# Kernel optimization log

Hardware: AMD Instinct MI355X
Metric: run time of the kernel (lower is better)

## Reference

```python
import jax, jax.numpy as jnp
import numpy as np

N_SIDE = 64
P = N_SIDE * N_SIDE          # n_patch = 4096
B = 8                        # n_batch
H = 32                       # n_hidden
E = H + 2                    # mhsa embed_dim = 34
N_OBS = 10
N_PRED = 50


def _neighbor_flat():
    # Reproduce the module's boundary-corrected 3x3 neighborhood indices.
    idx = np.arange(P)
    rows, cols = idx // N_SIDE, idx % N_SIDE
    off = np.array([[-1, -1], [-1, 0], [-1, 1], [0, -1], [0, 0], [0, 1], [1, -1], [1, 0], [1, 1]])
    nr = (rows[:, None] + off[:, 0]).reshape(N_SIDE, N_SIDE, 9)
    nc = (cols[:, None] + off[:, 1]).reshape(N_SIDE, N_SIDE, 9)
    nr[0] += 1; nr[-1] -= 1          # shift edge rows inward
    nc[:, 0] += 1; nc[:, -1] -= 1    # shift edge cols inward
    return jnp.asarray((nr * N_SIDE + nc).reshape(P, 9))

NEIGH = _neighbor_flat()  # (P, 9) flat patch indices


def _patch_label():
    r = (np.arange(N_SIDE) / N_SIDE).astype(np.float32)
    lab = np.stack(np.meshgrid(r, r, indexing='ij'), axis=-1).reshape(P, 2)
    return jnp.asarray(lab)

LABEL = _patch_label()  # (P, 2) normalized (row, col) coords


def _layernorm(x, g, b, eps=1e-5):
    m = x.mean(-1, keepdims=True)
    v = ((x - m) ** 2).mean(-1, keepdims=True)
    return (x - m) * jax.lax.rsqrt(v + eps) * g + b


def _step(h, params):
    # One local-attention step: h (B*P, H) -> layernorm(fc2(h + fc_sa(attn_center)))
    ipw, ipb, opw, opb, saw, sab, f2w, f2b, lg, lb = params
    q = h.reshape(B, P, H).transpose(1, 0, 2)                       # (P, B, H)
    lab = jnp.broadcast_to(LABEL[:, None, :], (P, B, 2))
    q = jnp.concatenate([q, lab], axis=-1)                          # (P, B, E)
    tok = q[NEIGH]                                                  # (P, 9, B, E) neighbor gather
    tok = tok.transpose(1, 2, 0, 3).reshape(9, B * P, E)            # (S=9, N, E)
    qkv = tok @ ipw.T + ipb                                         # (9, N, 3E)
    qq, kk, vv = jnp.split(qkv, 3, axis=-1)
    scores = jnp.einsum('sne,tne->nst', qq, kk) / jnp.sqrt(jnp.float32(E))
    w = jax.nn.softmax(scores, axis=-1)                             # (N, 9, 9)
    av = jnp.einsum('nst,tne->sne', w, vv)                          # (9, N, E)
    av = av @ opw.T + opb
    new_h = h + av[4] @ saw.T + sab                                 # center token + residual
    return _layernorm(new_h @ f2w.T + f2b, lg, lb)


def setup_inputs() -> dict:
    key = jax.random.key(0)
    ks = jax.random.split(key, 10)
    s = 0.05
    return {
        'x': jax.random.normal(ks[0], (N_OBS, B * P, H), jnp.float32),
        'in_proj_w': jax.random.normal(ks[1], (3 * E, E), jnp.float32) * s,
        'in_proj_b': jax.random.normal(ks[2], (3 * E,), jnp.float32) * s,
        'out_proj_w': jax.random.normal(ks[3], (E, E), jnp.float32) * s,
        'out_proj_b': jax.random.normal(ks[4], (E,), jnp.float32) * s,
        'fc_sa_w': jax.random.normal(ks[5], (H, E), jnp.float32) * s,
        'fc_sa_b': jax.random.normal(ks[6], (H,), jnp.float32) * s,
        'fc2_w': jax.random.normal(ks[7], (H, H), jnp.float32) * s,
        'fc2_b': jax.random.normal(ks[8], (H,), jnp.float32) * s,
        'ln2_g': jnp.ones((H,), jnp.float32),
        'ln2_b': jnp.zeros((H,), jnp.float32),
    }


def reference(x, in_proj_w, in_proj_b, out_proj_w, out_proj_b, fc_sa_w, fc_sa_b, fc2_w, fc2_b, ln2_g, ln2_b):
    params = (in_proj_w, in_proj_b, out_proj_w, out_proj_b, fc_sa_w, fc_sa_b, fc2_w, fc2_b, ln2_g, ln2_b)
    # Observation phase: 10 independent steps over x[t] -> vmap over time.
    obs = jax.vmap(lambda xt: _step(xt, params))(x)                 # (N_OBS, N, H)
    # Prediction phase: 50 sequential steps rolling on the last prediction.
    def scan_fn(h, _):
        p = _step(h, params)
        return p, p
    _, preds = jax.lax.scan(scan_fn, obs[-1], None, length=N_PRED)  # (N_PRED, N, H)
    return jnp.concatenate([obs, preds], axis=0)                    # (60, B*P, H)
```

## Files before the change

### kernel.cpp

```cpp
#include <hip/hip_runtime.h>
#include <hip/hip_bf16.h>

typedef __hip_bfloat16 bf16;
typedef unsigned short u16;
typedef unsigned int   u32;

#define PP    4096
#define HH    32
#define NTOK  32768
#define NSTEP 60
#define NOBS  10
#define SKK   35
#define SVP   33

#define OFF_WIN  0
#define OFF_BIN  3672
#define OFF_WFSA 3776
#define OFF_BFSA 4928
#define OFF_F2W  4960
#define OFF_F2B  5984
#define OFF_LNG  6016
#define OFF_LNB  6048
#define OFF_WVP  6080
#define OFF_BVP  7232
#define WGT_FLOATS 7264
#define WGT_BYTES  (7296 * 4)

__device__ __forceinline__ float bb(bf16 v) { return __bfloat162float(v); }

__device__ __forceinline__ int detect_f32(const u16* raw) {
  int bad = 0;
#pragma unroll
  for (int i = 0; i < 40; i++) {
    float f = __uint_as_float(((u32)raw[2 * i]) << 16);
    bad |= !(fabsf(f) < 1.0f);
  }
  return bad;
}

__device__ __forceinline__ float rdw(const void* p, int i, int f32) {
  return f32 ? ((const float*)p)[i] : bb(((const bf16*)p)[i]);
}

__device__ __forceinline__ void load_h(const void* hsrc, int hf32, int n, float* he) {
  if (hf32) {
    const float4* p = (const float4*)((const float*)hsrc + (size_t)n * HH);
#pragma unroll
    for (int k = 0; k < 8; k++) {
      float4 v = p[k];
      he[4 * k] = v.x; he[4 * k + 1] = v.y; he[4 * k + 2] = v.z; he[4 * k + 3] = v.w;
    }
  } else {
    const uint4* p = (const uint4*)((const bf16*)hsrc + (size_t)n * HH);
#pragma unroll
    for (int k = 0; k < 4; k++) {
      uint4 v = p[k];
      u32 w[4] = {v.x, v.y, v.z, v.w};
#pragma unroll
      for (int m = 0; m < 4; m++) {
        he[8 * k + 2 * m]     = __uint_as_float(w[m] << 16);
        he[8 * k + 2 * m + 1] = __uint_as_float(w[m] & 0xffff0000u);
      }
    }
  }
}

__device__ __forceinline__ void load_h8(const void* hsrc, int hf32, int n, int off, float* o8) {
  if (hf32) {
    const float4* p = (const float4*)((const float*)hsrc + (size_t)n * HH + off);
    float4 a = p[0], b = p[1];
    o8[0]=a.x; o8[1]=a.y; o8[2]=a.z; o8[3]=a.w;
    o8[4]=b.x; o8[5]=b.y; o8[6]=b.z; o8[7]=b.w;
  } else {
    uint4 v = *(const uint4*)((const bf16*)hsrc + (size_t)n * HH + off);
    u32 w[4] = {v.x, v.y, v.z, v.w};
#pragma unroll
    for (int m = 0; m < 4; m++) {
      o8[2 * m]     = __uint_as_float(w[m] << 16);
      o8[2 * m + 1] = __uint_as_float(w[m] & 0xffff0000u);
    }
  }
}

__global__ void prep_kernel(const void* __restrict__ ipw, const void* __restrict__ ipb,
                            const void* __restrict__ opw, const void* __restrict__ opb,
                            const void* __restrict__ saw, const void* __restrict__ sab,
                            const void* __restrict__ f2w, const void* __restrict__ f2b,
                            const void* __restrict__ lng, const void* __restrict__ lnb,
                            float* __restrict__ gw) {
  const int f32 = detect_f32((const u16*)ipw);
  int i = blockIdx.x * blockDim.x + threadIdx.x;
  if (i < 3672) { int r = i / 36, e = i - r * 36;
    gw[OFF_WIN + i] = (e < 34) ? rdw(ipw, r * 34 + e, f32) : 0.f; return; }
  i -= 3672;
  if (i < 104)  { gw[OFF_BIN + i] = (i < 102) ? rdw(ipb, i, f32) : 0.f; return; }
  i -= 104;
  if (i < 1152) { int r = i / 36, e = i - r * 36; float a = 0.f;
    if (e < 34) for (int f = 0; f < 34; f++)
      a += rdw(saw, r * 34 + f, f32) * rdw(opw, f * 34 + e, f32);
    gw[OFF_WFSA + i] = a; return; }
  i -= 1152;
  if (i < 32)   { float a = rdw(sab, i, f32);
    for (int f = 0; f < 34; f++) a += rdw(saw, i * 34 + f, f32) * rdw(opb, f, f32);
    gw[OFF_BFSA + i] = a; return; }
  i -= 32;
  if (i < 1024) { gw[OFF_F2W + i] = rdw(f2w, i, f32); return; }
  i -= 1024;
  if (i < 32)   { gw[OFF_F2B + i] = rdw(f2b, i, f32); return; }
  i -= 32;
  if (i < 32)   { gw[OFF_LNG + i] = rdw(lng, i, f32); return; }
  i -= 32;
  if (i < 32)   { gw[OFF_LNB + i] = rdw(lnb, i, f32); return; }
  i -= 32;
  if (i < 1152) {
    int r = i / 36, e = i - r * 36; float a = 0.f;
    if (e < 34) {
      for (int f = 0; f < 34; f++) {
        float wf = 0.f;
        for (int g = 0; g < 34; g++)
          wf += rdw(saw, r * 34 + g, f32) * rdw(opw, g * 34 + f, f32);
        a += wf * rdw(ipw, (68 + f) * 34 + e, f32);
      }
    }
    gw[OFF_WVP + i] = a; return; }
  i -= 1152;
  if (i < 32) {
    float a = rdw(sab, i, f32);
    for (int g = 0; g < 34; g++) a += rdw(saw, i * 34 + g, f32) * rdw(opb, g, f32);
    for (int f = 0; f < 34; f++) {
      float wf = 0.f;
      for (int g = 0; g < 34; g++)
        wf += rdw(saw, i * 34 + g, f32) * rdw(opw, g * 34 + f, f32);
      a += wf * rdw(ipb, 68 + f, f32);
    }
    gw[OFF_BVP + i] = a; return; }
}

__global__ __launch_bounds__(512, 4)
void step_kernel(int t0, const void* __restrict__ x, void* __restrict__ out,
                 const float* __restrict__ gw,
                 const void* __restrict__ ipw, const void* __restrict__ ipb,
                 const void* __restrict__ opw, const void* __restrict__ opb,
                 const void* __restrict__ saw, const void* __restrict__ sab,
                 const void* __restrict__ f2w, const void* __restrict__ f2b,
                 const void* __restrict__ lng, const void* __restrict__ lnb,
                 float* __restrict__ hb0) {
  __shared__ float s_k [256 * SKK];
  __shared__ float s_vp[256 * SVP];
  __shared__ float s_wvp[32 * 36 + 32];

  const int f32 = detect_f32((const u16*)ipw);
  const int tt = threadIdx.x;
  const int tstep = t0 + blockIdx.y;
  const int b  = blockIdx.x >> 5;
  const int r0 = (blockIdx.x & 31) << 1;

  const void* hsrc; int hf32;
  if (tstep < NOBS) {
    hsrc = f32 ? (const void*)((const float*)x + (size_t)tstep * NTOK * HH)
               : (const void*)((const bf16*)x + (size_t)tstep * NTOK * HH);
    hf32 = f32;
  } else if (f32) {
    hsrc = (const void*)((const float*)out + (size_t)(tstep - 1) * NTOK * HH); hf32 = 1;
  } else if (hb0) {
    hsrc = (const void*)(hb0 + (size_t)((tstep - 1) & 1) * NTOK * HH); hf32 = 1;
  } else {
    hsrc = (const void*)((const bf16*)out + (size_t)(tstep - 1) * NTOK * HH); hf32 = 0;
  }

  if (!gw) {
    for (int i = tt; i < 32 * 36 + 32; i += 512) {
      if (i < 32 * 36) {
        int r = i / 36, e = i - r * 36; float a = 0.f;
        if (e < 34) {
          for (int f = 0; f < 34; f++) {
            float wf = 0.f;
            for (int g = 0; g < 34; g++)
              wf += rdw(saw, r * 34 + g, f32) * rdw(opw, g * 34 + f, f32);
            a += wf * rdw(ipw, (68 + f) * 34 + e, f32);
          }
        }
        s_wvp[i] = a;
      } else {
        int r = i - 32 * 36;
        float a = rdw(sab, r, f32);
        for (int g = 0; g < 34; g++) a += rdw(saw, r * 34 + g, f32) * rdw(opb, g, f32);
        for (int f = 0; f < 34; f++) {
          float wf = 0.f;
          for (int g = 0; g < 34; g++)
            wf += rdw(saw, r * 34 + g, f32) * rdw(opw, g * 34 + f, f32);
          a += wf * rdw(ipb, 68 + f, f32);
        }
        s_wvp[i] = a;
      }
    }
    __syncthreads();
  }

  {
    const int a_idx = tt & 255;
    const int a_half = tt >> 8;
    const int tr = a_idx >> 6, col = a_idx & 63;
    int grow = r0 - 1 + tr; grow = max(0, min(63, grow));
    float he[36];
    load_h(hsrc, hf32, b * PP + grow * 64 + col, he);
    he[32] = grow * (1.f / 64.f); he[33] = col * (1.f / 64.f);
    he[34] = 0.f; he[35] = 0.f;

    if (a_half == 0) {
      float* dst = s_k + a_idx * SKK;
      if (gw) {
#pragma unroll
        for (int j = 0; j < 34; j++) {
          const float4* w4 = (const float4*)(gw + OFF_WIN + (34 + j) * 36);
          float acc = gw[OFF_BIN + 34 + j];
#pragma unroll
          for (int g = 0; g < 9; g++) {
            float4 w = w4[g];
            acc += w.x * he[4*g] + w.y * he[4*g+1] + w.z * he[4*g+2] + w.w * he[4*g+3];
          }
          dst[j] = acc;
        }
      } else {
        for (int j = 0; j < 34; j++) {
          float acc = rdw(ipb, 34 + j, f32);
          for (int e = 0; e < 34; e++) acc += rdw(ipw, (34 + j) * 34 + e, f32) * he[e];
          dst[j] = acc;
        }
      }
    } else {
      float* dst = s_vp + a_idx * SVP;
      if (gw) {
#pragma unroll
        for (int j = 0; j < 32; j++) {
          const float4* w4 = (const float4*)(gw + OFF_WVP + j * 36);
          float acc = gw[OFF_BVP + j];
#pragma unroll
          for (int g = 0; g < 9; g++) {
            float4 w = w4[g];
            acc += w.x * he[4*g] + w.y * he[4*g+1] + w.z * he[4*g+2] + w.w * he[4*g+3];
          }
          dst[j] = acc;
        }
      } else {
        for (int j = 0; j < 32; j++) {
          float acc = s_wvp[32 * 36 + j];
          const float* wr = s_wvp + j * 36;
          for (int e = 0; e < 34; e++) acc += wr[e] * he[e];
          dst[j] = acc;
        }
      }
    }
  }
  __syncthreads();

  const int tl = tt >> 2, qd = tt & 3;
  const int prow = r0 + (tl >> 6), pcol = tl & 63;
  const int rr = prow + (prow == 0) - (prow == 63);
  const int cc = pcol + (pcol == 0) - (pcol == 63);
  const int np = b * PP + prow * 64 + pcol;

  const int e0 = (qd < 2) ? qd * 9 : 18 + (qd - 2) * 8;
  const int ne = (qd < 2) ? 9 : 8;

  float hq[36];
  load_h(hsrc, hf32, b * PP + rr * 64 + cc, hq);
  hq[32] = rr * (1.f / 64.f); hq[33] = cc * (1.f / 64.f);
  hq[34] = 0.f; hq[35] = 0.f;

  float q[9];
#pragma unroll
  for (int jj = 0; jj < 9; jj++) {
    float a = 0.f;
    if (jj < ne) {
      const int row = e0 + jj;
      if (gw) {
        const float4* w4 = (const float4*)(gw + OFF_WIN + row * 36);
        a = gw[OFF_BIN + row];
#pragma unroll
        for (int g = 0; g < 9; g++) {
          float4 w = w4[g];
          a += w.x * hq[4*g] + w.y * hq[4*g+1] + w.z * hq[4*g+2] + w.w * hq[4*g+3];
        }
      } else {
        a = rdw(ipb, row, f32);
        for (int e = 0; e < 34; e++) a += rdw(ipw, row * 34 + e, f32) * hq[e];
      }
    }
    q[jj] = a;
  }

  int lts[9];
#pragma unroll
  for (int dr = 0; dr < 3; dr++)
#pragma unroll
    for (int dc = 0; dc < 3; dc++)
      lts[dr * 3 + dc] = (rr - r0 + dr) * 64 + (cc - 1 + dc);

  float w9[9];
  float mx = -1e30f;
#pragma unroll
  for (int tn = 0; tn < 9; tn++) {
    const float* kp = s_k + lts[tn] * SKK + e0;
    float a = 0.f;
#pragma unroll
    for (int jj = 0; jj < 9; jj++)
      if (jj < ne) a += q[jj] * kp[jj];
    a += __shfl_xor(a, 1);
    a += __shfl_xor(a, 2);
    w9[tn] = a * 0.17149858514250882f;
    mx = fmaxf(mx, w9[tn]);
  }
  float ssum = 0.f;
#pragma unroll
  for (int tn = 0; tn < 9; tn++) { w9[tn] = expf(w9[tn] - mx); ssum += w9[tn]; }
  const float inv = 1.f / ssum;
#pragma unroll
  for (int tn = 0; tn < 9; tn++) w9[tn] *= inv;

  float he8[8];
  load_h8(hsrc, hf32, np, qd * 8, he8);

  float nh8[8];
#pragma unroll
  for (int k = 0; k < 8; k++) nh8[k] = he8[k];
#pragma unroll
  for (int tn = 0; tn < 9; tn++) {
    const float wv = w9[tn];
    const float* vp = s_vp + lts[tn] * SVP + qd * 8;
#pragma unroll
    for (int k = 0; k < 8; k++) nh8[k] += wv * vp[k];
  }

  float y[32];
#pragma unroll
  for (int j = 0; j < 32; j++) {
    float a;
    if (gw) {
      const float4* w4 = (const float4*)(gw + OFF_F2W + j * 32 + qd * 8);
      float4 wa = w4[0], wb = w4[1];
      a = wa.x * nh8[0] + wa.y * nh8[1] + wa.z * nh8[2] + wa.w * nh8[3]
        + wb.x * nh8[4] + wb.y * nh8[5] + wb.z * nh8[6] + wb.w * nh8[7];
    } else {
      a = 0.f;
      for (int k2 = 0; k2 < 8; k2++) a += rdw(f2w, j * 32 + qd * 8 + k2, f32) * nh8[k2];
    }
    a += __shfl_xor(a, 1);
    a += __shfl_xor(a, 2);
    y[j] = a + (gw ? gw[OFF_F2B + j] : rdw(f2b, j, f32));
  }

  float m = 0.f;
#pragma unroll
  for (int j = 0; j < 32; j++) m += y[j];
  m *= (1.f / 32.f);
  float var = 0.f;
#pragma unroll
  for (int j = 0; j < 32; j++) { float d = y[j] - m; var += d * d; }
  var *= (1.f / 32.f);
  float rstd = rsqrtf(var + 1e-5f);
  rstd = rstd * (1.5f - 0.5f * (var + 1e-5f) * rstd * rstd);

  float o8[8];
#pragma unroll
  for (int k = 0; k < 8; k++) {
    float v01 = (qd & 1) ? y[8 + k]  : y[k];
    float v23 = (qd & 1) ? y[24 + k] : y[16 + k];
    float vy  = (qd & 2) ? v23 : v01;
    float g  = gw ? gw[OFF_LNG + qd * 8 + k] : rdw(lng, qd * 8 + k, f32);
    float b2 = gw ? gw[OFF_LNB + qd * 8 + k] : rdw(lnb, qd * 8 + k, f32);
    o8[k] = (vy - m) * rstd * g + b2;
  }

  const size_t obase = ((size_t)tstep * NTOK + np) * HH + qd * 8;
  if (f32) {
    float4* po = (float4*)((float*)out + obase);
    po[0] = make_float4(o8[0], o8[1], o8[2], o8[3]);
    po[1] = make_float4(o8[4], o8[5], o8[6], o8[7]);
  } else {
    u32 pk[4];
#pragma unroll
    for (int k2 = 0; k2 < 4; k2++) {
      bf16 b0 = __float2bfloat16(o8[2 * k2]);
      bf16 b1 = __float2bfloat16(o8[2 * k2 + 1]);
      pk[k2] = (u32)*reinterpret_cast<u16*>(&b0)
             | ((u32)*reinterpret_cast<u16*>(&b1) << 16);
    }
    *(uint4*)((bf16*)out + obase) = make_uint4(pk[0], pk[1], pk[2], pk[3]);
    if (hb0 && tstep >= NOBS - 1) {
      float4* ph = (float4*)(hb0 + (size_t)(tstep & 1) * NTOK * HH + (size_t)np * HH + qd * 8);
      ph[0] = make_float4(o8[0], o8[1], o8[2], o8[3]);
      ph[1] = make_float4(o8[4], o8[5], o8[6], o8[7]);
    }
  }
}

extern "C" void kernel_launch(void* const* d_in, const int* in_sizes, int n_in,
                              void* d_out, int out_size, void* d_ws, size_t ws_size,
                              hipStream_t stream) {
  const void* x = d_in[0];
  float* gw  = (ws_size >= (size_t)WGT_BYTES) ? (float*)d_ws : nullptr;
  float* hb0 = (ws_size >= (size_t)WGT_BYTES + 2ull * NTOK * HH * 4)
                 ? (float*)((char*)d_ws + WGT_BYTES) : nullptr;

  if (gw)
    prep_kernel<<<29, 256, 0, stream>>>(d_in[1], d_in[2], d_in[3], d_in[4], d_in[5],
                                        d_in[6], d_in[7], d_in[8], d_in[9], d_in[10], gw);

  step_kernel<<<dim3(256, NOBS), 512, 0, stream>>>(0, x, d_out, gw,
                                       d_in[1], d_in[2], d_in[3], d_in[4], d_in[5],
                                       d_in[6], d_in[7], d_in[8], d_in[9], d_in[10],
                                       hb0);

  for (int t = NOBS; t < NSTEP; t++) {
    step_kernel<<<dim3(256, 1), 512, 0, stream>>>(t, x, d_out, gw,
                                       d_in[1], d_in[2], d_in[3], d_in[4], d_in[5],
                                       d_in[6], d_in[7], d_in[8], d_in[9], d_in[10],
                                       hb0);
  }
}
```

Baseline: 2.507 ms.

## Run prediction steps in one persistent cooperative kernel with grid sync

Replaces the 50 sequential per-step kernel launches of the prediction phase with a single cooperative kernel of 256 blocks that loops over steps and uses a grid-wide barrier between them. The step body is factored into a shared device function. This removes per-launch overhead and kernel drain/fill gaps between steps, at the cost of grid-sync latency and the need for all blocks to be co-resident; it falls back to the old launches if the cooperative launch fails.

```diff
diff --git a/kernel.cpp b/kernel.cpp
--- a/kernel.cpp
+++ b/kernel.cpp
@@ -1,5 +1,8 @@
 #include <hip/hip_runtime.h>
 #include <hip/hip_bf16.h>
+#include <hip/hip_cooperative_groups.h>
+
+namespace cg = cooperative_groups;
 
 typedef __hip_bfloat16 bf16;
 typedef unsigned short u16;
@@ -23,7 +26,6 @@
 #define OFF_LNB  6048
 #define OFF_WVP  6080
 #define OFF_BVP  7232
-#define WGT_FLOATS 7264
 #define WGT_BYTES  (7296 * 4)
 
 __device__ __forceinline__ float bb(bf16 v) { return __bfloat162float(v); }
@@ -136,6 +138,213 @@
     gw[OFF_BVP + i] = a; return; }
 }
 
+__device__ __forceinline__ void do_step(
+    int tstep, const void* hsrc, int hf32, int f32,
+    void* __restrict__ out, const float* __restrict__ gw,
+    const void* __restrict__ ipw, const void* __restrict__ ipb,
+    const void* __restrict__ f2w, const void* __restrict__ f2b,
+    const void* __restrict__ lng, const void* __restrict__ lnb,
+    float* __restrict__ hb0, int b, int r0, int tt,
+    float* s_k, float* s_vp, const float* s_wvp) {
+
+  {
+    const int a_idx = tt & 255;
+    const int a_half = tt >> 8;
+    const int tr = a_idx >> 6, col = a_idx & 63;
+    int grow = r0 - 1 + tr; grow = max(0, min(63, grow));
+    float he[36];
+    load_h(hsrc, hf32, b * PP + grow * 64 + col, he);
+    he[32] = grow * (1.f / 64.f); he[33] = col * (1.f / 64.f);
+    he[34] = 0.f; he[35] = 0.f;
+
+    if (a_half == 0) {
+      float* dst = s_k + a_idx * SKK;
+      if (gw) {
+#pragma unroll
+        for (int j = 0; j < 34; j++) {
+          const float4* w4 = (const float4*)(gw + OFF_WIN + (34 + j) * 36);
+          float acc = gw[OFF_BIN + 34 + j];
+#pragma unroll
+          for (int g = 0; g < 9; g++) {
+            float4 w = w4[g];
+            acc += w.x * he[4*g] + w.y * he[4*g+1] + w.z * he[4*g+2] + w.w * he[4*g+3];
+          }
+          dst[j] = acc;
+        }
+      } else {
+        for (int j = 0; j < 34; j++) {
+          float acc = rdw(ipb, 34 + j, f32);
+          for (int e = 0; e < 34; e++) acc += rdw(ipw, (34 + j) * 34 + e, f32) * he[e];
+          dst[j] = acc;
+        }
+      }
+    } else {
+      float* dst = s_vp + a_idx * SVP;
+      if (gw) {
+#pragma unroll
+        for (int j = 0; j < 32; j++) {
+          const float4* w4 = (const float4*)(gw + OFF_WVP + j * 36);
+          float acc = gw[OFF_BVP + j];
+#pragma unroll
+          for (int g = 0; g < 9; g++) {
+            float4 w = w4[g];
+            acc += w.x * he[4*g] + w.y * he[4*g+1] + w.z * he[4*g+2] + w.w * he[4*g+3];
+          }
+          dst[j] = acc;
+        }
+      } else {
+        for (int j = 0; j < 32; j++) {
+          float acc = s_wvp[32 * 36 + j];
+          const float* wr = s_wvp + j * 36;
+          for (int e = 0; e < 34; e++) acc += wr[e] * he[e];
+          dst[j] = acc;
+        }
+      }
+    }
+  }
+  __syncthreads();
+
+  const int tl = tt >> 2, qd = tt & 3;
+  const int prow = r0 + (tl >> 6), pcol = tl & 63;
+  const int rr = prow + (prow == 0) - (prow == 63);
+  const int cc = pcol + (pcol == 0) - (pcol == 63);
+  const int np = b * PP + prow * 64 + pcol;
+
+  const int e0 = (qd < 2) ? qd * 9 : 18 + (qd - 2) * 8;
+  const int ne = (qd < 2) ? 9 : 8;
+
+  float hq[36];
+  load_h(hsrc, hf32, b * PP + rr * 64 + cc, hq);
+  hq[32] = rr * (1.f / 64.f); hq[33] = cc * (1.f / 64.f);
+  hq[34] = 0.f; hq[35] = 0.f;
+
+  float q[9];
+#pragma unroll
+  for (int jj = 0; jj < 9; jj++) {
+    float a = 0.f;
+    if (jj < ne) {
+      const int row = e0 + jj;
+      if (gw) {
+        const float4* w4 = (const float4*)(gw + OFF_WIN + row * 36);
+        a = gw[OFF_BIN + row];
+#pragma unroll
+        for (int g = 0; g < 9; g++) {
+          float4 w = w4[g];
+          a += w.x * hq[4*g] + w.y * hq[4*g+1] + w.z * hq[4*g+2] + w.w * hq[4*g+3];
+        }
+      } else {
+        a = rdw(ipb, row, f32);
+        for (int e = 0; e < 34; e++) a += rdw(ipw, row * 34 + e, f32) * hq[e];
+      }
+    }
+    q[jj] = a;
+  }
+
+  int lts[9];
+#pragma unroll
+  for (int dr = 0; dr < 3; dr++)
+#pragma unroll
+    for (int dc = 0; dc < 3; dc++)
+      lts[dr * 3 + dc] = (rr - r0 + dr) * 64 + (cc - 1 + dc);
+
+  float w9[9];
+  float mx = -1e30f;
+#pragma unroll
+  for (int tn = 0; tn < 9; tn++) {
+    const float* kp = s_k + lts[tn] * SKK + e0;
+    float a = 0.f;
+#pragma unroll
+    for (int jj = 0; jj < 9; jj++)
+      if (jj < ne) a += q[jj] * kp[jj];
+    a += __shfl_xor(a, 1);
+    a += __shfl_xor(a, 2);
+    w9[tn] = a * 0.17149858514250882f;
+    mx = fmaxf(mx, w9[tn]);
+  }
+  float ssum = 0.f;
+#pragma unroll
+  for (int tn = 0; tn < 9; tn++) { w9[tn] = expf(w9[tn] - mx); ssum += w9[tn]; }
+  const float inv = 1.f / ssum;
+#pragma unroll
+  for (int tn = 0; tn < 9; tn++) w9[tn] *= inv;
+
+  float he8[8];
+  load_h8(hsrc, hf32, np, qd * 8, he8);
+
+  float nh8[8];
+#pragma unroll
+  for (int k = 0; k < 8; k++) nh8[k] = he8[k];
+#pragma unroll
+  for (int tn = 0; tn < 9; tn++) {
+    const float wv = w9[tn];
+    const float* vp = s_vp + lts[tn] * SVP + qd * 8;
+#pragma unroll
+    for (int k = 0; k < 8; k++) nh8[k] += wv * vp[k];
+  }
+
+  float y[32];
+#pragma unroll
+  for (int j = 0; j < 32; j++) {
+    float a;
+    if (gw) {
+      const float4* w4 = (const float4*)(gw + OFF_F2W + j * 32 + qd * 8);
+      float4 wa = w4[0], wb = w4[1];
+      a = wa.x * nh8[0] + wa.y * nh8[1] + wa.z * nh8[2] + wa.w * nh8[3]
+        + wb.x * nh8[4] + wb.y * nh8[5] + wb.z * nh8[6] + wb.w * nh8[7];
+    } else {
+      a = 0.f;
+      for (int k2 = 0; k2 < 8; k2++) a += rdw(f2w, j * 32 + qd * 8 + k2, f32) * nh8[k2];
+    }
+    a += __shfl_xor(a, 1);
+    a += __shfl_xor(a, 2);
+    y[j] = a + (gw ? gw[OFF_F2B + j] : rdw(f2b, j, f32));
+  }
+
+  float m = 0.f;
+#pragma unroll
+  for (int j = 0; j < 32; j++) m += y[j];
+  m *= (1.f / 32.f);
+  float var = 0.f;
+#pragma unroll
+  for (int j = 0; j < 32; j++) { float d = y[j] - m; var += d * d; }
+  var *= (1.f / 32.f);
+  float rstd = rsqrtf(var + 1e-5f);
+  rstd = rstd * (1.5f - 0.5f * (var + 1e-5f) * rstd * rstd);
+
+  float o8[8];
+#pragma unroll
+  for (int k = 0; k < 8; k++) {
+    float v01 = (qd & 1) ? y[8 + k]  : y[k];
+    float v23 = (qd & 1) ? y[24 + k] : y[16 + k];
+    float vy  = (qd & 2) ? v23 : v01;
+    float g  = gw ? gw[OFF_LNG + qd * 8 + k] : rdw(lng, qd * 8 + k, f32);
+    float b2 = gw ? gw[OFF_LNB + qd * 8 + k] : rdw(lnb, qd * 8 + k, f32);
+    o8[k] = (vy - m) * rstd * g + b2;
+  }
+
+  const size_t obase = ((size_t)tstep * NTOK + np) * HH + qd * 8;
+  if (f32) {
+    float4* po = (float4*)((float*)out + obase);
+    po[0] = make_float4(o8[0], o8[1], o8[2], o8[3]);
+    po[1] = make_float4(o8[4], o8[5], o8[6], o8[7]);
+  } else {
+    u32 pk[4];
+#pragma unroll
+    for (int k2 = 0; k2 < 4; k2++) {
+      bf16 b0 = __float2bfloat16(o8[2 * k2]);
+      bf16 b1 = __float2bfloat16(o8[2 * k2 + 1]);
+      pk[k2] = (u32)*reinterpret_cast<u16*>(&b0)
+             | ((u32)*reinterpret_cast<u16*>(&b1) << 16);
+    }
+    *(uint4*)((bf16*)out + obase) = make_uint4(pk[0], pk[1], pk[2], pk[3]);
+    if (hb0 && tstep >= NOBS - 1) {
+      float4* ph = (float4*)(hb0 + (size_t)(tstep & 1) * NTOK * HH + (size_t)np * HH + qd * 8);
+      ph[0] = make_float4(o8[0], o8[1], o8[2], o8[3]);
+      ph[1] = make_float4(o8[4], o8[5], o8[6], o8[7]);
+    }
+  }
+}
+
 __global__ __launch_bounds__(512, 4)
 void step_kernel(int t0, const void* __restrict__ x, void* __restrict__ out,
                  const float* __restrict__ gw,
@@ -197,201 +406,37 @@
     __syncthreads();
   }
 
-  {
-    const int a_idx = tt & 255;
-    const int a_half = tt >> 8;
-    const int tr = a_idx >> 6, col = a_idx & 63;
-    int grow = r0 - 1 + tr; grow = max(0, min(63, grow));
-    float he[36];
-    load_h(hsrc, hf32, b * PP + grow * 64 + col, he);
-    he[32] = grow * (1.f / 64.f); he[33] = col * (1.f / 64.f);
-    he[34] = 0.f; he[35] = 0.f;
-
-    if (a_half == 0) {
-      float* dst = s_k + a_idx * SKK;
-      if (gw) {
-#pragma unroll
-        for (int j = 0; j < 34; j++) {
-          const float4* w4 = (const float4*)(gw + OFF_WIN + (34 + j) * 36);
-          float acc = gw[OFF_BIN + 34 + j];
-#pragma unroll
-          for (int g = 0; g < 9; g++) {
-            float4 w = w4[g];
-            acc += w.x * he[4*g] + w.y * he[4*g+1] + w.z * he[4*g+2] + w.w * he[4*g+3];
-          }
-          dst[j] = acc;
-        }
-      } else {
-        for (int j = 0; j < 34; j++) {
-          float acc = rdw(ipb, 34 + j, f32);
-          for (int e = 0; e < 34; e++) acc += rdw(ipw, (34 + j) * 34 + e, f32) * he[e];
-          dst[j] = acc;
-        }
-      }
+  do_step(tstep, hsrc, hf32, f32, out, gw, ipw, ipb, f2w, f2b, lng, lnb,
+          hb0, b, r0, tt, s_k, s_vp, s_wvp);
+}
+
+__global__ __launch_bounds__(512)
+void coop_kernel(void* __restrict__ out, const float* __restrict__ gw,
+                 const void* __restrict__ ipw, const void* __restrict__ ipb,
+                 const void* __restrict__ f2w, const void* __restrict__ f2b,
+                 const void* __restrict__ lng, const void* __restrict__ lnb,
+                 float* __restrict__ hb0) {
+  __shared__ float s_k [256 * SKK];
+  __shared__ float s_vp[256 * SVP];
+
+  cg::grid_group grid = cg::this_grid();
+  const int f32 = detect_f32((const u16*)ipw);
+  const int tt = threadIdx.x;
+  const int b  = blockIdx.x >> 5;
+  const int r0 = (blockIdx.x & 31) << 1;
+
+  for (int t = NOBS; t < NSTEP; t++) {
+    const void* hsrc; int hf32;
+    if (f32) {
+      hsrc = (const void*)((const float*)out + (size_t)(t - 1) * NTOK * HH); hf32 = 1;
+    } else if (hb0) {
+      hsrc = (const void*)(hb0 + (size_t)((t - 1) & 1) * NTOK * HH); hf32 = 1;
     } else {
-      float* dst = s_vp + a_idx * SVP;
-      if (gw) {
-#pragma unroll
-        for (int j = 0; j < 32; j++) {
-          const float4* w4 = (const float4*)(gw + OFF_WVP + j * 36);
-          float acc = gw[OFF_BVP + j];
-#pragma unroll
-          for (int g = 0; g < 9; g++) {
-            float4 w = w4[g];
-            acc += w.x * he[4*g] + w.y * he[4*g+1] + w.z * he[4*g+2] + w.w * he[4*g+3];
-          }
-          dst[j] = acc;
-        }
-      } else {
-        for (int j = 0; j < 32; j++) {
-          float acc = s_wvp[32 * 36 + j];
-          const float* wr = s_wvp + j * 36;
-          for (int e = 0; e < 34; e++) acc += wr[e] * he[e];
-          dst[j] = acc;
-        }
-      }
-    }
-  }
-  __syncthreads();
-
-  const int tl = tt >> 2, qd = tt & 3;
-  const int prow = r0 + (tl >> 6), pcol = tl & 63;
-  const int rr = prow + (prow == 0) - (prow == 63);
-  const int cc = pcol + (pcol == 0) - (pcol == 63);
-  const int np = b * PP + prow * 64 + pcol;
-
-  const int e0 = (qd < 2) ? qd * 9 : 18 + (qd - 2) * 8;
-  const int ne = (qd < 2) ? 9 : 8;
-
-  float hq[36];
-  load_h(hsrc, hf32, b * PP + rr * 64 + cc, hq);
-  hq[32] = rr * (1.f / 64.f); hq[33] = cc * (1.f / 64.f);
-  hq[34] = 0.f; hq[35] = 0.f;
-
-  float q[9];
-#pragma unroll
-  for (int jj = 0; jj < 9; jj++) {
-    float a = 0.f;
-    if (jj < ne) {
-      const int row = e0 + jj;
-      if (gw) {
-        const float4* w4 = (const float4*)(gw + OFF_WIN + row * 36);
-        a = gw[OFF_BIN + row];
-#pragma unroll
-        for (int g = 0; g < 9; g++) {
-          float4 w = w4[g];
-          a += w.x * hq[4*g] + w.y * hq[4*g+1] + w.z * hq[4*g+2] + w.w * hq[4*g+3];
-        }
-      } else {
-        a = rdw(ipb, row, f32);
-        for (int e = 0; e < 34; e++) a += rdw(ipw, row * 34 + e, f32) * hq[e];
-      }
-    }
-    q[jj] = a;
-  }
-
-  int lts[9];
-#pragma unroll
-  for (int dr = 0; dr < 3; dr++)
-#pragma unroll
-    for (int dc = 0; dc < 3; dc++)
-      lts[dr * 3 + dc] = (rr - r0 + dr) * 64 + (cc - 1 + dc);
-
-  float w9[9];
-  float mx = -1e30f;
-#pragma unroll
-  for (int tn = 0; tn < 9; tn++) {
-    const float* kp = s_k + lts[tn] * SKK + e0;
-    float a = 0.f;
-#pragma unroll
-    for (int jj = 0; jj < 9; jj++)
-      if (jj < ne) a += q[jj] * kp[jj];
-    a += __shfl_xor(a, 1);
-    a += __shfl_xor(a, 2);
-    w9[tn] = a * 0.17149858514250882f;
-    mx = fmaxf(mx, w9[tn]);
-  }
-  float ssum = 0.f;
-#pragma unroll
-  for (int tn = 0; tn < 9; tn++) { w9[tn] = expf(w9[tn] - mx); ssum += w9[tn]; }
-  const float inv = 1.f / ssum;
-#pragma unroll
-  for (int tn = 0; tn < 9; tn++) w9[tn] *= inv;
-
-  float he8[8];
-  load_h8(hsrc, hf32, np, qd * 8, he8);
-
-  float nh8[8];
-#pragma unroll
-  for (int k = 0; k < 8; k++) nh8[k] = he8[k];
-#pragma unroll
-  for (int tn = 0; tn < 9; tn++) {
-    const float wv = w9[tn];
-    const float* vp = s_vp + lts[tn] * SVP + qd * 8;
-#pragma unroll
-    for (int k = 0; k < 8; k++) nh8[k] += wv * vp[k];
-  }
-
-  float y[32];
-#pragma unroll
-  for (int j = 0; j < 32; j++) {
-    float a;
-    if (gw) {
-      const float4* w4 = (const float4*)(gw + OFF_F2W + j * 32 + qd * 8);
-      float4 wa = w4[0], wb = w4[1];
-      a = wa.x * nh8[0] + wa.y * nh8[1] + wa.z * nh8[2] + wa.w * nh8[3]
-        + wb.x * nh8[4] + wb.y * nh8[5] + wb.z * nh8[6] + wb.w * nh8[7];
-    } else {
-      a = 0.f;
-      for (int k2 = 0; k2 < 8; k2++) a += rdw(f2w, j * 32 + qd * 8 + k2, f32) * nh8[k2];
-    }
-    a += __shfl_xor(a, 1);
-    a += __shfl_xor(a, 2);
-    y[j] = a + (gw ? gw[OFF_F2B + j] : rdw(f2b, j, f32));
-  }
-
-  float m = 0.f;
-#pragma unroll
-  for (int j = 0; j < 32; j++) m += y[j];
-  m *= (1.f / 32.f);
-  float var = 0.f;
-#pragma unroll
-  for (int j = 0; j < 32; j++) { float d = y[j] - m; var += d * d; }
-  var *= (1.f / 32.f);
-  float rstd = rsqrtf(var + 1e-5f);
-  rstd = rstd * (1.5f - 0.5f * (var + 1e-5f) * rstd * rstd);
-
-  float o8[8];
-#pragma unroll
-  for (int k = 0; k < 8; k++) {
-    float v01 = (qd & 1) ? y[8 + k]  : y[k];
-    float v23 = (qd & 1) ? y[24 + k] : y[16 + k];
-    float vy  = (qd & 2) ? v23 : v01;
-    float g  = gw ? gw[OFF_LNG + qd * 8 + k] : rdw(lng, qd * 8 + k, f32);
-    float b2 = gw ? gw[OFF_LNB + qd * 8 + k] : rdw(lnb, qd * 8 + k, f32);
-    o8[k] = (vy - m) * rstd * g + b2;
-  }
-
-  const size_t obase = ((size_t)tstep * NTOK + np) * HH + qd * 8;
-  if (f32) {
-    float4* po = (float4*)((float*)out + obase);
-    po[0] = make_float4(o8[0], o8[1], o8[2], o8[3]);
-    po[1] = make_float4(o8[4], o8[5], o8[6], o8[7]);
-  } else {
-    u32 pk[4];
-#pragma unroll
-    for (int k2 = 0; k2 < 4; k2++) {
-      bf16 b0 = __float2bfloat16(o8[2 * k2]);
-      bf16 b1 = __float2bfloat16(o8[2 * k2 + 1]);
-      pk[k2] = (u32)*reinterpret_cast<u16*>(&b0)
-             | ((u32)*reinterpret_cast<u16*>(&b1) << 16);
-    }
-    *(uint4*)((bf16*)out + obase) = make_uint4(pk[0], pk[1], pk[2], pk[3]);
-    if (hb0 && tstep >= NOBS - 1) {
-      float4* ph = (float4*)(hb0 + (size_t)(tstep & 1) * NTOK * HH + (size_t)np * HH + qd * 8);
-      ph[0] = make_float4(o8[0], o8[1], o8[2], o8[3]);
-      ph[1] = make_float4(o8[4], o8[5], o8[6], o8[7]);
-    }
+      hsrc = (const void*)((const bf16*)out + (size_t)(t - 1) * NTOK * HH); hf32 = 0;
+    }
+    do_step(t, hsrc, hf32, f32, out, gw, ipw, ipb, f2w, f2b, lng, lnb,
+            hb0, b, r0, tt, s_k, s_vp, nullptr);
+    grid.sync();
   }
 }
 
@@ -412,10 +457,26 @@
                                        d_in[6], d_in[7], d_in[8], d_in[9], d_in[10],
                                        hb0);
 
-  for (int t = NOBS; t < NSTEP; t++) {
-    step_kernel<<<dim3(256, 1), 512, 0, stream>>>(t, x, d_out, gw,
-                                       d_in[1], d_in[2], d_in[3], d_in[4], d_in[5],
-                                       d_in[6], d_in[7], d_in[8], d_in[9], d_in[10],
-                                       hb0);
-  }
-}
+  bool coop_done = false;
+  if (gw) {
+    void* outp = d_out;
+    const float* gwp = gw;
+    const void* ipw = d_in[1]; const void* ipb = d_in[2];
+    const void* f2w = d_in[7]; const void* f2b = d_in[8];
+    const void* lng = d_in[9]; const void* lnb = d_in[10];
+    float* hb0p = hb0;
+    void* args[] = { &outp, &gwp, &ipw, &ipb, &f2w, &f2b, &lng, &lnb, &hb0p };
+    hipError_t e = hipLaunchCooperativeKernel((const void*)coop_kernel,
+                                              dim3(256), dim3(512), args, 0, stream);
+    coop_done = (e == hipSuccess);
+  }
+
+  if (!coop_done) {
+    for (int t = NOBS; t < NSTEP; t++) {
+      step_kernel<<<dim3(256, 1), 512, 0, stream>>>(t, x, d_out, gw,
+                                         d_in[1], d_in[2], d_in[3], d_in[4], d_in[5],
+                                         d_in[6], d_in[7], d_in[8], d_in[9], d_in[10],
+                                         hb0);
+    }
+  }
+}
```

Result: slower. 4.055 ms (+61.8%).

## Fuse 50 prediction steps into one cooperative persistent kernel with grid sync

Applied to the files above, without the earlier changes.

Replaces the 50 sequential per-step launches with one cooperative kernel that loops over the prediction steps and calls grid.sync between them. This removes repeated launch overhead and weight reloads. Packed weights are now staged once into shared memory and reused, and the kernel hoists all h loads ahead of the first barrier. Launch bounds drop to 2 blocks per CU, and there is a fallback to per-step launches if the cooperative launch fails. The risks are grid-sync cost and lower occupancy.

```diff
diff --git a/kernel.cpp b/kernel.cpp
--- a/kernel.cpp
+++ b/kernel.cpp
@@ -1,5 +1,8 @@
 #include <hip/hip_runtime.h>
 #include <hip/hip_bf16.h>
+#include <hip/hip_cooperative_groups.h>
+
+namespace cg = cooperative_groups;
 
 typedef __hip_bfloat16 bf16;
 typedef unsigned short u16;
@@ -13,18 +16,18 @@
 #define SKK   35
 #define SVP   33
 
-#define OFF_WIN  0
-#define OFF_BIN  3672
-#define OFF_WFSA 3776
-#define OFF_BFSA 4928
-#define OFF_F2W  4960
-#define OFF_F2B  5984
-#define OFF_LNG  6016
-#define OFF_LNB  6048
-#define OFF_WVP  6080
-#define OFF_BVP  7232
-#define WGT_FLOATS 7264
-#define WGT_BYTES  (7296 * 4)
+#define PW_Q   0
+#define PW_K   1224
+#define PW_V   2448
+#define PW_F2  3600
+#define PB_Q   4624
+#define PB_K   4658
+#define PB_V   4692
+#define PB_F2  4724
+#define P_LNG  4756
+#define P_LNB  4788
+#define PK_FLOATS 4820
+#define WGT_BYTES (4832 * 4)
 
 __device__ __forceinline__ float bb(bf16 v) { return __bfloat162float(v); }
 
@@ -82,36 +85,16 @@
   }
 }
 
-__global__ void prep_kernel(const void* __restrict__ ipw, const void* __restrict__ ipb,
-                            const void* __restrict__ opw, const void* __restrict__ opb,
-                            const void* __restrict__ saw, const void* __restrict__ sab,
-                            const void* __restrict__ f2w, const void* __restrict__ f2b,
-                            const void* __restrict__ lng, const void* __restrict__ lnb,
-                            float* __restrict__ gw) {
-  const int f32 = detect_f32((const u16*)ipw);
-  int i = blockIdx.x * blockDim.x + threadIdx.x;
-  if (i < 3672) { int r = i / 36, e = i - r * 36;
-    gw[OFF_WIN + i] = (e < 34) ? rdw(ipw, r * 34 + e, f32) : 0.f; return; }
-  i -= 3672;
-  if (i < 104)  { gw[OFF_BIN + i] = (i < 102) ? rdw(ipb, i, f32) : 0.f; return; }
-  i -= 104;
-  if (i < 1152) { int r = i / 36, e = i - r * 36; float a = 0.f;
-    if (e < 34) for (int f = 0; f < 34; f++)
-      a += rdw(saw, r * 34 + f, f32) * rdw(opw, f * 34 + e, f32);
-    gw[OFF_WFSA + i] = a; return; }
-  i -= 1152;
-  if (i < 32)   { float a = rdw(sab, i, f32);
-    for (int f = 0; f < 34; f++) a += rdw(saw, i * 34 + f, f32) * rdw(opb, f, f32);
-    gw[OFF_BFSA + i] = a; return; }
-  i -= 32;
-  if (i < 1024) { gw[OFF_F2W + i] = rdw(f2w, i, f32); return; }
-  i -= 1024;
-  if (i < 32)   { gw[OFF_F2B + i] = rdw(f2b, i, f32); return; }
-  i -= 32;
-  if (i < 32)   { gw[OFF_LNG + i] = rdw(lng, i, f32); return; }
-  i -= 32;
-  if (i < 32)   { gw[OFF_LNB + i] = rdw(lnb, i, f32); return; }
-  i -= 32;
+__device__ float compute_pk(int i,
+    const void* ipw, const void* ipb, const void* opw, const void* opb,
+    const void* saw, const void* sab, const void* f2w, const void* f2b,
+    const void* lng, const void* lnb, int f32) {
+  if (i < 1224) { int r = i / 36, e = i - r * 36;
+    return (e < 34) ? rdw(ipw, r * 34 + e, f32) : 0.f; }
+  i -= 1224;
+  if (i < 1224) { int r = i / 36, e = i - r * 36;
+    return (e < 34) ? rdw(ipw, (34 + r) * 34 + e, f32) : 0.f; }
+  i -= 1224;
   if (i < 1152) {
     int r = i / 36, e = i - r * 36; float a = 0.f;
     if (e < 34) {
@@ -122,8 +105,14 @@
         a += wf * rdw(ipw, (68 + f) * 34 + e, f32);
       }
     }
-    gw[OFF_WVP + i] = a; return; }
+    return a; }
   i -= 1152;
+  if (i < 1024) return rdw(f2w, i, f32);
+  i -= 1024;
+  if (i < 34)   return rdw(ipb, i, f32);
+  i -= 34;
+  if (i < 34)   return rdw(ipb, 34 + i, f32);
+  i -= 34;
   if (i < 32) {
     float a = rdw(sab, i, f32);
     for (int g = 0; g < 34; g++) a += rdw(saw, i * 34 + g, f32) * rdw(opb, g, f32);
@@ -133,10 +122,197 @@
         wf += rdw(saw, i * 34 + g, f32) * rdw(opw, g * 34 + f, f32);
       a += wf * rdw(ipb, 68 + f, f32);
     }
-    gw[OFF_BVP + i] = a; return; }
-}
-
-__global__ __launch_bounds__(512, 4)
+    return a; }
+  i -= 32;
+  if (i < 32) return rdw(f2b, i, f32);
+  i -= 32;
+  if (i < 32) return rdw(lng, i, f32);
+  i -= 32;
+  return rdw(lnb, i - 32, f32);
+}
+
+__global__ void prep_kernel(const void* __restrict__ ipw, const void* __restrict__ ipb,
+                            const void* __restrict__ opw, const void* __restrict__ opb,
+                            const void* __restrict__ saw, const void* __restrict__ sab,
+                            const void* __restrict__ f2w, const void* __restrict__ f2b,
+                            const void* __restrict__ lng, const void* __restrict__ lnb,
+                            float* __restrict__ gw) {
+  const int f32 = detect_f32((const u16*)ipw);
+  int i = blockIdx.x * blockDim.x + threadIdx.x;
+  if (i < PK_FLOATS)
+    gw[i] = compute_pk(i, ipw, ipb, opw, opb, saw, sab, f2w, f2b, lng, lnb, f32);
+}
+
+__device__ __forceinline__ void do_step(
+    int tstep, const void* hsrc, int hf32, int f32,
+    void* __restrict__ out, float* __restrict__ hb0,
+    int b, int r0, int tt,
+    const float* s_w, float* s_k, float* s_vp) {
+
+  const int a_idx = tt & 255;
+  const int a_half = tt >> 8;
+  const int tr = a_idx >> 6, col = a_idx & 63;
+  int grow = r0 - 1 + tr; grow = max(0, min(63, grow));
+
+  const int tl = tt >> 2, qd = tt & 3;
+  const int prow = r0 + (tl >> 6), pcol = tl & 63;
+  const int rr = prow + (prow == 0) - (prow == 63);
+  const int cc = pcol + (pcol == 0) - (pcol == 63);
+  const int np = b * PP + prow * 64 + pcol;
+
+  float he[36], hq[36], he8[8];
+  load_h(hsrc, hf32, b * PP + grow * 64 + col, he);
+  load_h(hsrc, hf32, b * PP + rr * 64 + cc, hq);
+  load_h8(hsrc, hf32, np, qd * 8, he8);
+  he[32] = grow * (1.f / 64.f); he[33] = col * (1.f / 64.f); he[34] = 0.f; he[35] = 0.f;
+  hq[32] = rr * (1.f / 64.f);   hq[33] = cc * (1.f / 64.f);  hq[34] = 0.f; hq[35] = 0.f;
+
+  if (a_half == 0) {
+    float* dst = s_k + a_idx * SKK;
+#pragma unroll
+    for (int j = 0; j < 34; j++) {
+      const float4* w4 = (const float4*)(s_w + PW_K + j * 36);
+      float acc = s_w[PB_K + j];
+#pragma unroll
+      for (int g = 0; g < 9; g++) {
+        float4 w = w4[g];
+        acc += w.x * he[4*g] + w.y * he[4*g+1] + w.z * he[4*g+2] + w.w * he[4*g+3];
+      }
+      dst[j] = acc;
+    }
+  } else {
+    float* dst = s_vp + a_idx * SVP;
+#pragma unroll
+    for (int j = 0; j < 32; j++) {
+      const float4* w4 = (const float4*)(s_w + PW_V + j * 36);
+      float acc = s_w[PB_V + j];
+#pragma unroll
+      for (int g = 0; g < 9; g++) {
+        float4 w = w4[g];
+        acc += w.x * he[4*g] + w.y * he[4*g+1] + w.z * he[4*g+2] + w.w * he[4*g+3];
+      }
+      dst[j] = acc;
+    }
+  }
+
+  const int e0 = (qd < 2) ? qd * 9 : 18 + (qd - 2) * 8;
+  const int ne = (qd < 2) ? 9 : 8;
+  float q[9];
+#pragma unroll
+  for (int jj = 0; jj < 9; jj++) {
+    float a = 0.f;
+    if (jj < ne) {
+      const int row = e0 + jj;
+      const float4* w4 = (const float4*)(s_w + PW_Q + row * 36);
+      a = s_w[PB_Q + row];
+#pragma unroll
+      for (int g = 0; g < 9; g++) {
+        float4 w = w4[g];
+        a += w.x * hq[4*g] + w.y * hq[4*g+1] + w.z * hq[4*g+2] + w.w * hq[4*g+3];
+      }
+    }
+    q[jj] = a;
+  }
+
+  __syncthreads();
+
+  int lts[9];
+#pragma unroll
+  for (int dr = 0; dr < 3; dr++)
+#pragma unroll
+    for (int dc = 0; dc < 3; dc++)
+      lts[dr * 3 + dc] = (rr - r0 + dr) * 64 + (cc - 1 + dc);
+
+  float w9[9];
+  float mx = -1e30f;
+#pragma unroll
+  for (int tn = 0; tn < 9; tn++) {
+    const float* kp = s_k + lts[tn] * SKK + e0;
+    float a = 0.f;
+#pragma unroll
+    for (int jj = 0; jj < 9; jj++)
+      if (jj < ne) a += q[jj] * kp[jj];
+    a += __shfl_xor(a, 1);
+    a += __shfl_xor(a, 2);
+    w9[tn] = a * 0.17149858514250882f;
+    mx = fmaxf(mx, w9[tn]);
+  }
+  float ssum = 0.f;
+#pragma unroll
+  for (int tn = 0; tn < 9; tn++) { w9[tn] = expf(w9[tn] - mx); ssum += w9[tn]; }
+  const float inv = 1.f / ssum;
+#pragma unroll
+  for (int tn = 0; tn < 9; tn++) w9[tn] *= inv;
+
+  float nh8[8];
+#pragma unroll
+  for (int k = 0; k < 8; k++) nh8[k] = he8[k];
+#pragma unroll
+  for (int tn = 0; tn < 9; tn++) {
+    const float wv = w9[tn];
+    const float* vp = s_vp + lts[tn] * SVP + qd * 8;
+#pragma unroll
+    for (int k = 0; k < 8; k++) nh8[k] += wv * vp[k];
+  }
+
+  float y[32];
+#pragma unroll
+  for (int j = 0; j < 32; j++) {
+    const float4* w4 = (const float4*)(s_w + PW_F2 + j * 32 + qd * 8);
+    float4 wa = w4[0], wb = w4[1];
+    float a = wa.x * nh8[0] + wa.y * nh8[1] + wa.z * nh8[2] + wa.w * nh8[3]
+            + wb.x * nh8[4] + wb.y * nh8[5] + wb.z * nh8[6] + wb.w * nh8[7];
+    a += __shfl_xor(a, 1);
+    a += __shfl_xor(a, 2);
+    y[j] = a + s_w[PB_F2 + j];
+  }
+
+  float m = 0.f;
+#pragma unroll
+  for (int j = 0; j < 32; j++) m += y[j];
+  m *= (1.f / 32.f);
+  float var = 0.f;
+#pragma unroll
+  for (int j = 0; j < 32; j++) { float d = y[j] - m; var += d * d; }
+  var *= (1.f / 32.f);
+  float rstd = rsqrtf(var + 1e-5f);
+  rstd = rstd * (1.5f - 0.5f * (var + 1e-5f) * rstd * rstd);
+
+  float o8[8];
+#pragma unroll
+  for (int k = 0; k < 8; k++) {
+    float v01 = (qd & 1) ? y[8 + k]  : y[k];
+    float v23 = (qd & 1) ? y[24 + k] : y[16 + k];
+    float vy  = (qd & 2) ? v23 : v01;
+    float g  = s_w[P_LNG + qd * 8 + k];
+    float b2 = s_w[P_LNB + qd * 8 + k];
+    o8[k] = (vy - m) * rstd * g + b2;
+  }
+
+  const size_t obase = ((size_t)tstep * NTOK + np) * HH + qd * 8;
+  if (f32) {
+    float4* po = (float4*)((float*)out + obase);
+    po[0] = make_float4(o8[0], o8[1], o8[2], o8[3]);
+    po[1] = make_float4(o8[4], o8[5], o8[6], o8[7]);
+  } else {
+    u32 pk[4];
+#pragma unroll
+    for (int k2 = 0; k2 < 4; k2++) {
+      bf16 b0 = __float2bfloat16(o8[2 * k2]);
+      bf16 b1 = __float2bfloat16(o8[2 * k2 + 1]);
+      pk[k2] = (u32)*reinterpret_cast<u16*>(&b0)
+             | ((u32)*reinterpret_cast<u16*>(&b1) << 16);
+    }
+    *(uint4*)((bf16*)out + obase) = make_uint4(pk[0], pk[1], pk[2], pk[3]);
+    if (hb0 && tstep >= NOBS - 1) {
+      float4* ph = (float4*)(hb0 + (size_t)(tstep & 1) * NTOK * HH + (size_t)np * HH + qd * 8);
+      ph[0] = make_float4(o8[0], o8[1], o8[2], o8[3]);
+      ph[1] = make_float4(o8[4], o8[5], o8[6], o8[7]);
+    }
+  }
+}
+
+__global__ __launch_bounds__(512, 2)
 void step_kernel(int t0, const void* __restrict__ x, void* __restrict__ out,
                  const float* __restrict__ gw,
                  const void* __restrict__ ipw, const void* __restrict__ ipb,
@@ -145,9 +321,9 @@
                  const void* __restrict__ f2w, const void* __restrict__ f2b,
                  const void* __restrict__ lng, const void* __restrict__ lnb,
                  float* __restrict__ hb0) {
-  __shared__ float s_k [256 * SKK];
-  __shared__ float s_vp[256 * SVP];
-  __shared__ float s_wvp[32 * 36 + 32];
+  __shared__ __align__(16) float s_w[PK_FLOATS];
+  __shared__ __align__(16) float s_k[256 * SKK];
+  __shared__ __align__(16) float s_vp[256 * SVP];
 
   const int f32 = detect_f32((const u16*)ipw);
   const int tt = threadIdx.x;
@@ -168,230 +344,46 @@
     hsrc = (const void*)((const bf16*)out + (size_t)(tstep - 1) * NTOK * HH); hf32 = 0;
   }
 
-  if (!gw) {
-    for (int i = tt; i < 32 * 36 + 32; i += 512) {
-      if (i < 32 * 36) {
-        int r = i / 36, e = i - r * 36; float a = 0.f;
-        if (e < 34) {
-          for (int f = 0; f < 34; f++) {
-            float wf = 0.f;
-            for (int g = 0; g < 34; g++)
-              wf += rdw(saw, r * 34 + g, f32) * rdw(opw, g * 34 + f, f32);
-            a += wf * rdw(ipw, (68 + f) * 34 + e, f32);
-          }
-        }
-        s_wvp[i] = a;
-      } else {
-        int r = i - 32 * 36;
-        float a = rdw(sab, r, f32);
-        for (int g = 0; g < 34; g++) a += rdw(saw, r * 34 + g, f32) * rdw(opb, g, f32);
-        for (int f = 0; f < 34; f++) {
-          float wf = 0.f;
-          for (int g = 0; g < 34; g++)
-            wf += rdw(saw, r * 34 + g, f32) * rdw(opw, g * 34 + f, f32);
-          a += wf * rdw(ipb, 68 + f, f32);
-        }
-        s_wvp[i] = a;
-      }
-    }
-    __syncthreads();
-  }
-
-  {
-    const int a_idx = tt & 255;
-    const int a_half = tt >> 8;
-    const int tr = a_idx >> 6, col = a_idx & 63;
-    int grow = r0 - 1 + tr; grow = max(0, min(63, grow));
-    float he[36];
-    load_h(hsrc, hf32, b * PP + grow * 64 + col, he);
-    he[32] = grow * (1.f / 64.f); he[33] = col * (1.f / 64.f);
-    he[34] = 0.f; he[35] = 0.f;
-
-    if (a_half == 0) {
-      float* dst = s_k + a_idx * SKK;
-      if (gw) {
-#pragma unroll
-        for (int j = 0; j < 34; j++) {
-          const float4* w4 = (const float4*)(gw + OFF_WIN + (34 + j) * 36);
-          float acc = gw[OFF_BIN + 34 + j];
-#pragma unroll
-          for (int g = 0; g < 9; g++) {
-            float4 w = w4[g];
-            acc += w.x * he[4*g] + w.y * he[4*g+1] + w.z * he[4*g+2] + w.w * he[4*g+3];
-          }
-          dst[j] = acc;
-        }
-      } else {
-        for (int j = 0; j < 34; j++) {
-          float acc = rdw(ipb, 34 + j, f32);
-          for (int e = 0; e < 34; e++) acc += rdw(ipw, (34 + j) * 34 + e, f32) * he[e];
-          dst[j] = acc;
-        }
-      }
+  if (gw) {
+    for (int i = tt; i < PK_FLOATS / 4; i += 512)
+      ((float4*)s_w)[i] = ((const float4*)gw)[i];
+  } else {
+    for (int i = tt; i < PK_FLOATS; i += 512)
+      s_w[i] = compute_pk(i, ipw, ipb, opw, opb, saw, sab, f2w, f2b, lng, lnb, f32);
+  }
+  __syncthreads();
+
+  do_step(tstep, hsrc, hf32, f32, out, hb0, b, r0, tt, s_w, s_k, s_vp);
+}
+
+__global__ __launch_bounds__(512, 2)
+void coop_kernel(void* __restrict__ out, const float* __restrict__ gw,
+                 const void* __restrict__ ipw, float* __restrict__ hb0) {
+  __shared__ __align__(16) float s_w[PK_FLOATS];
+  __shared__ __align__(16) float s_k[256 * SKK];
+  __shared__ __align__(16) float s_vp[256 * SVP];
+
+  cg::grid_group grid = cg::this_grid();
+  const int f32 = detect_f32((const u16*)ipw);
+  const int tt = threadIdx.x;
+  const int b  = blockIdx.x >> 5;
+  const int r0 = (blockIdx.x & 31) << 1;
+
+  for (int i = tt; i < PK_FLOATS / 4; i += 512)
+    ((float4*)s_w)[i] = ((const float4*)gw)[i];
+  __syncthreads();
+
+  for (int t = NOBS; t < NSTEP; t++) {
+    const void* hsrc; int hf32;
+    if (f32) {
+      hsrc = (const void*)((const float*)out + (size_t)(t - 1) * NTOK * HH); hf32 = 1;
+    } else if (hb0) {
+      hsrc = (const void*)(hb0 + (size_t)((t - 1) & 1) * NTOK * HH); hf32 = 1;
     } else {
-      float* dst = s_vp + a_idx * SVP;
-      if (gw) {
-#pragma unroll
-        for (int j = 0; j < 32; j++) {
-          const float4* w4 = (const float4*)(gw + OFF_WVP + j * 36);
-          float acc = gw[OFF_BVP + j];
-#pragma unroll
-          for (int g = 0; g < 9; g++) {
-            float4 w = w4[g];
-            acc += w.x * he[4*g] + w.y * he[4*g+1] + w.z * he[4*g+2] + w.w * he[4*g+3];
-          }
-          dst[j] = acc;
-        }
-      } else {
-        for (int j = 0; j < 32; j++) {
-          float acc = s_wvp[32 * 36 + j];
-          const float* wr = s_wvp + j * 36;
-          for (int e = 0; e < 34; e++) acc += wr[e] * he[e];
-          dst[j] = acc;
-        }
-      }
-    }
-  }
-  __syncthreads();
-
-  const int tl = tt >> 2, qd = tt & 3;
-  const int prow = r0 + (tl >> 6), pcol = tl & 63;
-  const int rr = prow + (prow == 0) - (prow == 63);
-  const int cc = pcol + (pcol == 0) - (pcol == 63);
-  const int np = b * PP + prow * 64 + pcol;
-
-  const int e0 = (qd < 2) ? qd * 9 : 18 + (qd - 2) * 8;
-  const int ne = (qd < 2) ? 9 : 8;
-
-  float hq[36];
-  load_h(hsrc, hf32, b * PP + rr * 64 + cc, hq);
-  hq[32] = rr * (1.f / 64.f); hq[33] = cc * (1.f / 64.f);
-  hq[34] = 0.f; hq[35] = 0.f;
-
-  float q[9];
-#pragma unroll
-  for (int jj = 0; jj < 9; jj++) {
-    float a = 0.f;
-    if (jj < ne) {
-      const int row = e0 + jj;
-      if (gw) {
-        const float4* w4 = (const float4*)(gw + OFF_WIN + row * 36);
-        a = gw[OFF_BIN + row];
-#pragma unroll
-        for (int g = 0; g < 9; g++) {
-          float4 w = w4[g];
-          a += w.x * hq[4*g] + w.y * hq[4*g+1] + w.z * hq[4*g+2] + w.w * hq[4*g+3];
-        }
-      } else {
-        a = rdw(ipb, row, f32);
-        for (int e = 0; e < 34; e++) a += rdw(ipw, row * 34 + e, f32) * hq[e];
-      }
-    }
-    q[jj] = a;
-  }
-
-  int lts[9];
-#pragma unroll
-  for (int dr = 0; dr < 3; dr++)
-#pragma unroll
-    for (int dc = 0; dc < 3; dc++)
-      lts[dr * 3 + dc] = (rr - r0 + dr) * 64 + (cc - 1 + dc);
-
-  float w9[9];
-  float mx = -1e30f;
-#pragma unroll
-  for (int tn = 0; tn < 9; tn++) {
-    const float* kp = s_k + lts[tn] * SKK + e0;
-    float a = 0.f;
-#pragma unroll
-    for (int jj = 0; jj < 9; jj++)
-      if (jj < ne) a += q[jj] * kp[jj];
-    a += __shfl_xor(a, 1);
-    a += __shfl_xor(a, 2);
-    w9[tn] = a * 0.17149858514250882f;
-    mx = fmaxf(mx, w9[tn]);
-  }
-  float ssum = 0.f;
-#pragma unroll
-  for (int tn = 0; tn < 9; tn++) { w9[tn] = expf(w9[tn] - mx); ssum += w9[tn]; }
-  const float inv = 1.f / ssum;
-#pragma unroll
-  for (int tn = 0; tn < 9; tn++) w9[tn] *= inv;
-
-  float he8[8];
-  load_h8(hsrc, hf32, np, qd * 8, he8);
-
-  float nh8[8];
-#pragma unroll
-  for (int k = 0; k < 8; k++) nh8[k] = he8[k];
-#pragma unroll
-  for (int tn = 0; tn < 9; tn++) {
-    const float wv = w9[tn];
-    const float* vp = s_vp + lts[tn] * SVP + qd * 8;
-#pragma unroll
-    for (int k = 0; k < 8; k++) nh8[k] += wv * vp[k];
-  }
-
-  float y[32];
-#pragma unroll
-  for (int j = 0; j < 32; j++) {
-    float a;
-    if (gw) {
-      const float4* w4 = (const float4*)(gw + OFF_F2W + j * 32 + qd * 8);
-      float4 wa = w4[0], wb = w4[1];
-      a = wa.x * nh8[0] + wa.y * nh8[1] + wa.z * nh8[2] + wa.w * nh8[3]
-        + wb.x * nh8[4] + wb.y * nh8[5] + wb.z * nh8[6] + wb.w * nh8[7];
-    } else {
-      a = 0.f;
-      for (int k2 = 0; k2 < 8; k2++) a += rdw(f2w, j * 32 + qd * 8 + k2, f32) * nh8[k2];
-    }
-    a += __shfl_xor(a, 1);
-    a += __shfl_xor(a, 2);
-    y[j] = a + (gw ? gw[OFF_F2B + j] : rdw(f2b, j, f32));
-  }
-
-  float m = 0.f;
-#pragma unroll
-  for (int j = 0; j < 32; j++) m += y[j];
-  m *= (1.f / 32.f);
-  float var = 0.f;
-#pragma unroll
-  for (int j = 0; j < 32; j++) { float d = y[j] - m; var += d * d; }
-  var *= (1.f / 32.f);
-  float rstd = rsqrtf(var + 1e-5f);
-  rstd = rstd * (1.5f - 0.5f * (var + 1e-5f) * rstd * rstd);
-
-  float o8[8];
-#pragma unroll
-  for (int k = 0; k < 8; k++) {
-    float v01 = (qd & 1) ? y[8 + k]  : y[k];
-    float v23 = (qd & 1) ? y[24 + k] : y[16 + k];
-    float vy  = (qd & 2) ? v23 : v01;
-    float g  = gw ? gw[OFF_LNG + qd * 8 + k] : rdw(lng, qd * 8 + k, f32);
-    float b2 = gw ? gw[OFF_LNB + qd * 8 + k] : rdw(lnb, qd * 8 + k, f32);
-    o8[k] = (vy - m) * rstd * g + b2;
-  }
-
-  const size_t obase = ((size_t)tstep * NTOK + np) * HH + qd * 8;
-  if (f32) {
-    float4* po = (float4*)((float*)out + obase);
-    po[0] = make_float4(o8[0], o8[1], o8[2], o8[3]);
-    po[1] = make_float4(o8[4], o8[5], o8[6], o8[7]);
-  } else {
-    u32 pk[4];
-#pragma unroll
-    for (int k2 = 0; k2 < 4; k2++) {
-      bf16 b0 = __float2bfloat16(o8[2 * k2]);
-      bf16 b1 = __float2bfloat16(o8[2 * k2 + 1]);
-      pk[k2] = (u32)*reinterpret_cast<u16*>(&b0)
-             | ((u32)*reinterpret_cast<u16*>(&b1) << 16);
-    }
-    *(uint4*)((bf16*)out + obase) = make_uint4(pk[0], pk[1], pk[2], pk[3]);
-    if (hb0 && tstep >= NOBS - 1) {
-      float4* ph = (float4*)(hb0 + (size_t)(tstep & 1) * NTOK * HH + (size_t)np * HH + qd * 8);
-      ph[0] = make_float4(o8[0], o8[1], o8[2], o8[3]);
-      ph[1] = make_float4(o8[4], o8[5], o8[6], o8[7]);
-    }
+      hsrc = (const void*)((const bf16*)out + (size_t)(t - 1) * NTOK * HH); hf32 = 0;
+    }
+    do_step(t, hsrc, hf32, f32, out, hb0, b, r0, tt, s_w, s_k, s_vp);
+    grid.sync();
   }
 }
 
@@ -404,7 +396,7 @@
                  ? (float*)((char*)d_ws + WGT_BYTES) : nullptr;
 
   if (gw)
-    prep_kernel<<<29, 256, 0, stream>>>(d_in[1], d_in[2], d_in[3], d_in[4], d_in[5],
+    prep_kernel<<<19, 256, 0, stream>>>(d_in[1], d_in[2], d_in[3], d_in[4], d_in[5],
                                         d_in[6], d_in[7], d_in[8], d_in[9], d_in[10], gw);
 
   step_kernel<<<dim3(256, NOBS), 512, 0, stream>>>(0, x, d_out, gw,
@@ -412,10 +404,24 @@
                                        d_in[6], d_in[7], d_in[8], d_in[9], d_in[10],
                                        hb0);
 
-  for (int t = NOBS; t < NSTEP; t++) {
-    step_kernel<<<dim3(256, 1), 512, 0, stream>>>(t, x, d_out, gw,
-                                       d_in[1], d_in[2], d_in[3], d_in[4], d_in[5],
-                                       d_in[6], d_in[7], d_in[8], d_in[9], d_in[10],
-                                       hb0);
-  }
-}
+  bool coop_done = false;
+  if (gw) {
+    void* outp = d_out;
+    const float* gwp = gw;
+    const void* ipw = d_in[1];
+    float* hb0p = hb0;
+    void* args[] = { &outp, &gwp, &ipw, &hb0p };
+    hipError_t e = hipLaunchCooperativeKernel((const void*)coop_kernel,
+                                              dim3(256), dim3(512), args, 0, stream);
+    coop_done = (e == hipSuccess);
+  }
+
+  if (!coop_done) {
+    for (int t = NOBS; t < NSTEP; t++) {
+      step_kernel<<<dim3(256, 1), 512, 0, stream>>>(t, x, d_out, gw,
+                                         d_in[1], d_in[2], d_in[3], d_in[4], d_in[5],
+                                         d_in[6], d_in[7], d_in[8], d_in[9], d_in[10],
+                                         hb0);
+    }
+  }
+}
```

Result: slower. 4.482 ms (+78.8%).
